# Optimization experiments

Measured on AMD Instinct MI355X. Metric: run time of the kernel, lower is better.

Reference implementation:

```python
import math
import jax, jax.numpy as jnp
import numpy as np

B, N, F, K = 4, 4096, 128, 32
EPS = 1e-8  # tsl.epsilon
TEMP0, TEMP_DECAY = 1.0, 0.99995


def setup_inputs() -> dict:
    key = jax.random.key(0)
    k1, k2, k3, k4 = jax.random.split(key, 4)
    emb = jax.random.normal(k1, (B, N, F), dtype=jnp.float32)
    adj = jax.random.uniform(k2, (B, N, N), dtype=jnp.float32)
    logits_param = jax.random.normal(k3, (N, K), dtype=jnp.float32)
    u = jax.random.uniform(k4, (B, N, K), dtype=jnp.float32, minval=1e-9, maxval=1.0)
    gumbel_noise = -jnp.log(-jnp.log(u))
    return {"emb": emb, "adj": adj, "logits_param": logits_param, "gumbel_noise": gumbel_noise}


def reference(emb, adj, logits_param, gumbel_noise):
    # temp decays on each get_temp() call in training mode (called twice per forward)
    t1 = max(TEMP0 * TEMP_DECAY, 0.05)
    t2 = max(t1 * TEMP_DECAY, 0.05)

    # ---- gumbel-softmax hard sample with straight-through estimator ----
    y_soft = jax.nn.softmax(logits_param[None] / t1 + gumbel_noise, axis=-1)  # [B,N,K]
    y_hard = jax.nn.one_hot(jnp.argmax(y_soft, axis=-1), K, dtype=y_soft.dtype)
    s_sample = jax.lax.stop_gradient(y_hard - y_soft) + y_soft + EPS  # [B,N,K]

    # ---- soft assignment for regularizers (unbatched [N,K]) ----
    s_soft = jax.nn.softmax(logits_param / t2, axis=-1)  # [N,K]

    # mincut_num = trace(s^T A s) per batch, without forming [K,K]
    As = jnp.einsum('bnm,mk->bnk', adj, s_soft)            # [B,N,K]
    mincut_num = jnp.einsum('nk,bnk->b', s_soft, As)       # [B]
    # mincut_den = trace(s^T D s): D is diag(deg) -> O(N*K) instead of diag_embed
    d_flat = adj.sum(axis=-1)                              # [B,N]
    mincut_den = jnp.einsum('bn,nk,nk->b', d_flat, s_soft, s_soft)
    mincut_loss = -jnp.mean(mincut_num / mincut_den)

    ss = s_soft.T @ s_soft                                 # [K,K]
    ortho_loss = jnp.linalg.norm(ss / jnp.linalg.norm(ss) - jnp.eye(K, dtype=ss.dtype) / math.sqrt(K))

    # ---- pooling ----
    out_emb = jnp.einsum('bnk,bnf->bkf', s_sample, emb)    # [B,K,F]
    As2 = jnp.einsum('bnm,bml->bnl', adj, s_sample)        # [B,N,K]
    out_adj = jnp.einsum('bnk,bnl->bkl', s_sample, As2)    # [B,K,K]

    out_adj = out_adj * (1.0 - jnp.eye(K, dtype=out_adj.dtype))  # zero diagonal
    d = jnp.sqrt(out_adj.sum(axis=-1, keepdims=True)) + EPS
    out_adj = out_adj / d / jnp.swapaxes(d, -1, -2)

    return out_emb, out_adj, s_sample, mincut_loss, ortho_loss
```

## Files before the change

kernel.cpp:

```cpp
#include <hip/hip_runtime.h>
#include <hip/hip_bf16.h>
#include <math.h>

#define B_ 4
#define N_ 4096
#define F_ 128
#define K_ 32
#define EPS_ 1e-8f

typedef __attribute__((ext_vector_type(8))) __bf16 bf16x8;
typedef __attribute__((ext_vector_type(4))) float f32x4;

#define WS_SSOFT   0
#define WS_SQ      131072
#define WS_SSP     135168
#define WS_WFS     200704
#define WS_WFH     266240
#define WS_OADJP   528384
#define WS_NUMDEN  1576960
#define WS_PEMB    1579008
#define WS_H       2627584

__global__ void k_pre(const float* __restrict__ logits, const float* __restrict__ gum,
                      float* __restrict__ s_soft, float* __restrict__ sq,
                      float* __restrict__ ssp, float* __restrict__ s_sample,
                      int* __restrict__ h, bf16x8* __restrict__ wfs,
                      bf16x8* __restrict__ wfh, float t1, float t2) {
  __shared__ float sl[64][33];
  __shared__ int hl[4][64];
  int t = threadIdx.x;
  int r = blockIdx.x;
  int n0 = r * 64;

  if (t < 64) {
    int n = n0 + t;
    float z[32];
    float mx = -1e30f;
    for (int k = 0; k < 32; ++k) { z[k] = logits[n*32+k] / t2; mx = fmaxf(mx, z[k]); }
    float s = 0.f;
    for (int k = 0; k < 32; ++k) { z[k] = expf(z[k]-mx); s += z[k]; }
    float sqa = 0.f;
    for (int k = 0; k < 32; ++k) {
      float v = z[k] / s;
      s_soft[n*32+k] = v;
      sl[t][k] = v;
      sqa += v*v;
    }
    sq[n] = sqa;
  }

  {
    int b = t >> 6, nn = t & 63;
    int n = n0 + nn;
    size_t i = (size_t)b * N_ + n;
    float z[32];
    float mx = -1e30f;
    for (int k = 0; k < 32; ++k) { z[k] = logits[n*32+k]/t1 + gum[i*32+k]; mx = fmaxf(mx, z[k]); }
    float s = 0.f;
    for (int k = 0; k < 32; ++k) { z[k] = expf(z[k]-mx); s += z[k]; }
    int am = 0; float best = -1.f;
    for (int k = 0; k < 32; ++k) { z[k] = z[k]/s; if (z[k] > best) { best = z[k]; am = k; } }
    for (int k = 0; k < 32; ++k) {
      float yh = (k==am) ? 1.f : 0.f;
      s_sample[i*32+k] = (yh - z[k]) + z[k] + EPS_;
    }
    h[i] = am;
    hl[b][nn] = am;
  }
  __syncthreads();

  for (int pp = 0; pp < 4; ++pp) {
    int p = pp*256 + t;
    int k = p >> 5, l = p & 31;
    float a = 0.f;
    for (int rr = 0; rr < 64; ++rr) a += sl[rr][k]*sl[rr][l];
    ssp[(size_t)r*1024 + p] = a;
  }

  {
    int lane = t & 63;
    int c = (t >> 6) & 1;
    int tts = t >> 7;
    int col = c*16 + (lane & 15);
    int lrow = tts*32 + (lane >> 4)*8;
    bf16x8 v;
    #pragma unroll
    for (int j = 0; j < 8; ++j) v[j] = (__bf16)sl[lrow+j][col];
    wfs[((size_t)(2*r + tts)*2 + c)*64 + lane] = v;
  }

  for (int it = 0; it < 4; ++it) {
    int p = it*256 + t;
    int lane = p & 63;
    int c = (p >> 6) & 1;
    int tts = (p >> 7) & 1;
    int b = p >> 8;
    int cc = c*16 + (lane & 15);
    int lrow = tts*32 + (lane >> 4)*8;
    bf16x8 v;
    #pragma unroll
    for (int j = 0; j < 8; ++j) v[j] = (__bf16)((hl[b][lrow+j] == cc) ? 1.f : 0.f);
    wfh[(((size_t)b*(N_/32) + 2*r + tts)*2 + c)*64 + lane] = v;
  }
}

#define NT(p) __builtin_nontemporal_load((const f32x4*)(p))

__launch_bounds__(256, 4)
__global__ void k_gemm(const float* __restrict__ adj, const float* __restrict__ emb,
                       const bf16x8* __restrict__ wfs, const bf16x8* __restrict__ wfh,
                       const float* __restrict__ s_soft, const float* __restrict__ sq,
                       const int* __restrict__ h, float* __restrict__ numden_p,
                       float* __restrict__ oadjp, float* __restrict__ pemb) {
  __shared__ float sh[4096];
  __shared__ float rn[4], rd[4];
  int t = threadIdx.x;
  int bid = blockIdx.x;

  if (bid < 256) {
    for (int i = t; i < 4096; i += 256) sh[i] = 0.f;
    __syncthreads();
    int b = bid >> 6;
    int n0 = (bid & 63) * 64;
    int f = t & 127, rr = t >> 7;
    for (int it = 0; it < 32; ++it) {
      int n = n0 + it*2 + rr;
      float v = emb[((size_t)b*N_ + n)*F_ + f];
      int hv = h[b*N_ + n];
      atomicAdd(&sh[hv*128 + f], v);
    }
    __syncthreads();
    for (int i = t; i < 4096; i += 256) pemb[(size_t)bid*4096 + i] = sh[i];
    return;
  }

  int gid = bid - 256;
  int w = t >> 6, l = t & 63;
  int lr = l & 15, lhi = l >> 4;
  int sp = gid & 7, r = (gid >> 3) & 31, b = gid >> 8;
  float* oal = sh;

  for (int i = t; i < 1024; i += 256) oal[i] = 0.f;
  __syncthreads();

  int row0 = r*128;
  int m0 = sp*512;
  int rowA = row0 + w*32 + lr;

  const float* pA0 = adj + (size_t)b*N_*N_ + (size_t)rowA*N_ + m0 + lhi*8;
  const float* pA1 = pA0 + (size_t)16*N_;
  const bf16x8* pws = wfs + (size_t)(m0 >> 5)*128 + l;
  const bf16x8* pwh = wfh + ((size_t)b*(N_/32) + (m0 >> 5))*128 + l;

  f32x4 acc00 = {0,0,0,0}, acc01 = {0,0,0,0}, acc02 = {0,0,0,0}, acc03 = {0,0,0,0};
  f32x4 acc10 = {0,0,0,0}, acc11 = {0,0,0,0}, acc12 = {0,0,0,0}, acc13 = {0,0,0,0};

  f32x4 a0lo = NT(pA0), a0hi = NT(pA0 + 4);
  f32x4 a1lo = NT(pA1), a1hi = NT(pA1 + 4);
  bf16x8 wc0 = pws[0], wc1 = pws[64], wc2 = pwh[0], wc3 = pwh[64];

  #pragma unroll 1
  for (int c = 0; c < 16; ++c) {
    f32x4 n0lo, n0hi, n1lo, n1hi;
    bf16x8 wn0, wn1, wn2, wn3;
    if (c < 15) {
      pA0 += 32; pA1 += 32; pws += 128; pwh += 128;
      n0lo = NT(pA0); n0hi = NT(pA0 + 4);
      n1lo = NT(pA1); n1hi = NT(pA1 + 4);
      wn0 = pws[0]; wn1 = pws[64]; wn2 = pwh[0]; wn3 = pwh[64];
    }
    bf16x8 fa0, fa1;
    #pragma unroll
    for (int j = 0; j < 4; ++j) {
      fa0[j]   = (__bf16)a0lo[j];
      fa0[j+4] = (__bf16)a0hi[j];
      fa1[j]   = (__bf16)a1lo[j];
      fa1[j+4] = (__bf16)a1hi[j];
    }
    acc00 = __builtin_amdgcn_mfma_f32_16x16x32_bf16(fa0, wc0, acc00, 0, 0, 0);
    acc01 = __builtin_amdgcn_mfma_f32_16x16x32_bf16(fa0, wc1, acc01, 0, 0, 0);
    acc02 = __builtin_amdgcn_mfma_f32_16x16x32_bf16(fa0, wc2, acc02, 0, 0, 0);
    acc03 = __builtin_amdgcn_mfma_f32_16x16x32_bf16(fa0, wc3, acc03, 0, 0, 0);
    acc10 = __builtin_amdgcn_mfma_f32_16x16x32_bf16(fa1, wc0, acc10, 0, 0, 0);
    acc11 = __builtin_amdgcn_mfma_f32_16x16x32_bf16(fa1, wc1, acc11, 0, 0, 0);
    acc12 = __builtin_amdgcn_mfma_f32_16x16x32_bf16(fa1, wc2, acc12, 0, 0, 0);
    acc13 = __builtin_amdgcn_mfma_f32_16x16x32_bf16(fa1, wc3, acc13, 0, 0, 0);
    if (c < 15) {
      a0lo = n0lo; a0hi = n0hi; a1lo = n1lo; a1hi = n1hi;
      wc0 = wn0; wc1 = wn1; wc2 = wn2; wc3 = wn3;
    }
  }

  float numacc = 0.f, denacc = 0.f;
  {
    f32x4 a0s[2] = {acc00, acc10}, a1s[2] = {acc01, acc11};
    f32x4 a2s[2] = {acc02, acc12}, a3s[2] = {acc03, acc13};
    int wrow0 = row0 + w*32;
    #pragma unroll
    for (int rt = 0; rt < 2; ++rt) {
      int rbase = wrow0 + rt*16 + lhi*4;
      #pragma unroll
      for (int i = 0; i < 4; ++i) {
        int row = rbase + i;
        float sqv = sq[row];
        int hv = h[b*N_ + row];
        numacc += a0s[rt][i] * s_soft[row*32 + lr];
        numacc += a1s[rt][i] * s_soft[row*32 + 16 + lr];
        float v2 = a2s[rt][i], v3 = a3s[rt][i];
        denacc += (v2 + v3) * sqv;
        atomicAdd(&oal[hv*32 + lr], v2);
        atomicAdd(&oal[hv*32 + 16 + lr], v3);
      }
    }
  }
  for (int off = 32; off; off >>= 1) {
    numacc += __shfl_down(numacc, off);
    denacc += __shfl_down(denacc, off);
  }
  if (l == 0) { rn[w] = numacc; rd[w] = denacc; }
  __syncthreads();
  if (t == 0) {
    numden_p[gid] = rn[0]+rn[1]+rn[2]+rn[3];
    numden_p[1024 + gid] = rd[0]+rd[1]+rd[2]+rd[3];
  }
  for (int i = t; i < 1024; i += 256) oadjp[(size_t)gid*1024 + i] = oal[i];
}

__global__ void k_post(const float* __restrict__ oadjp, const float* __restrict__ pemb,
                       const float* __restrict__ ndp, const float* __restrict__ ssp,
                       float* __restrict__ dout) {
  int blk = blockIdx.x;
  int t = threadIdx.x;
  if (blk < 64) {
    int i = blk*256 + t;
    int b = i >> 12, ii = i & 4095;
    float s = 0.f;
    const float* p = pemb + (size_t)(b*64)*4096 + ii;
    for (int j = 0; j < 64; ++j) s += p[(size_t)j*4096];
    dout[i] = s;
  } else if (blk < 68) {
    __shared__ float oal[1024];
    __shared__ float dsh[32];
    int b = blk - 64;
    float a0 = 0.f, a1 = 0.f, a2 = 0.f, a3 = 0.f;
    const float* p = oadjp + (size_t)b*256*1024 + t;
    for (int j = 0; j < 256; ++j) {
      a0 += p[0]; a1 += p[256]; a2 += p[512]; a3 += p[768];
      p += 1024;
    }
    oal[t] = a0; oal[t+256] = a1; oal[t+512] = a2; oal[t+768] = a3;
    __syncthreads();
    if (t < 32) {
      float s = 0.f;
      for (int l = 0; l < 32; ++l) if (l != t) s += oal[t*32+l];
      dsh[t] = sqrtf(s) + EPS_;
    }
    __syncthreads();
    for (int i = t; i < 1024; i += 256) {
      int k = i >> 5, l = i & 31;
      float v = (k == l) ? 0.f : oal[i] / (dsh[k] * dsh[l]);
      dout[16384 + b*1024 + i] = v;
    }
  } else {
    __shared__ float red[256];
    __shared__ float nd[8];
    if (t < 8) {
      int b = t & 3;
      const float* p = ndp + (t >> 2)*1024 + b*256;
      float s = 0.f;
      for (int j = 0; j < 256; ++j) s += p[j];
      nd[t] = s;
    }
    float v0 = 0.f, v1 = 0.f, v2 = 0.f, v3 = 0.f;
    for (int r = 0; r < 64; ++r) {
      const float* p = ssp + (size_t)r*1024 + t;
      v0 += p[0]; v1 += p[256]; v2 += p[512]; v3 += p[768];
    }
    float a = v0*v0 + v1*v1 + v2*v2 + v3*v3;
    red[t] = a; __syncthreads();
    for (int s2 = 128; s2; s2 >>= 1) { if (t < s2) red[t] += red[t+s2]; __syncthreads(); }
    float fro = sqrtf(red[0]);
    __syncthreads();
    float inv = 1.f / fro;
    float dk = (float)(1.0 / sqrt(32.0));
    float c = 0.f;
    {
      float w;
      int p0 = t, p1 = t+256, p2 = t+512, p3 = t+768;
      w = v0*inv - (((p0>>5)==(p0&31)) ? dk : 0.f); c += w*w;
      w = v1*inv - (((p1>>5)==(p1&31)) ? dk : 0.f); c += w*w;
      w = v2*inv - (((p2>>5)==(p2&31)) ? dk : 0.f); c += w*w;
      w = v3*inv - (((p3>>5)==(p3&31)) ? dk : 0.f); c += w*w;
    }
    red[t] = c; __syncthreads();
    for (int s2 = 128; s2; s2 >>= 1) { if (t < s2) red[t] += red[t+s2]; __syncthreads(); }
    if (t == 0) {
      dout[544769] = sqrtf(red[0]);
      float s = 0.f;
      for (int b = 0; b < 4; ++b) s += nd[b] / nd[4+b];
      dout[544768] = -s*0.25f;
    }
  }
}

extern "C" void kernel_launch(void* const* d_in, const int* in_sizes, int n_in,
                              void* d_out, int out_size, void* d_ws, size_t ws_size,
                              hipStream_t stream) {
  const float* emb    = (const float*)d_in[0];
  const float* adj    = (const float*)d_in[1];
  const float* logits = (const float*)d_in[2];
  const float* gum    = (const float*)d_in[3];
  float* out = (float*)d_out;
  float* ws  = (float*)d_ws;

  float t1 = 0.99995f;
  float t2 = (float)(0.99995 * 0.99995);

  float* s_soft = ws + WS_SSOFT;
  float* sq     = ws + WS_SQ;
  float* ssp    = ws + WS_SSP;
  bf16x8* wfs   = (bf16x8*)(ws + WS_WFS);
  bf16x8* wfh   = (bf16x8*)(ws + WS_WFH);
  float* oadjp  = ws + WS_OADJP;
  float* ndp    = ws + WS_NUMDEN;
  float* pemb   = ws + WS_PEMB;
  int* hbuf     = (int*)(ws + WS_H);

  k_pre  <<<64, 256, 0, stream>>>(logits, gum, s_soft, sq, ssp, out + 20480, hbuf, wfs, wfh, t1, t2);
  k_gemm <<<1280, 256, 0, stream>>>(adj, emb, wfs, wfh, s_soft, sq, hbuf, ndp, oadjp, pemb);
  k_post <<<69, 256, 0, stream>>>(oadjp, pemb, ndp, ssp, out);
}
```

Before: 416.8 us.

## Stage adj tiles through swizzled LDS with full-row blocks and split-K across waves

The GEMM blocks now each own 32 full rows of adj. Threads load 32 contiguous floats per row with coalesced nontemporal loads, convert them to bf16, and write them into an XOR-swizzled shared-memory tile. Each wave then reads its K-slice of that tile as MFMA fragments. This replaces the earlier scheme, where each lane fetched 8-float fragments straight from global memory across 8 column splits. The aim is better-coalesced, deeper-prefetched streaming of the large adj matrix and fewer partial outputs to reduce in k_post. In exchange it adds two barriers per step, more registers (launch bounds lowered to 3), and fewer blocks (512 GEMM blocks instead of 1024).

Result: slower. 448.3 us (+7.6%).

```diff
diff --git a/kernel.cpp b/kernel.cpp
--- a/kernel.cpp
+++ b/kernel.cpp
@@ -10,6 +10,7 @@
 
 typedef __attribute__((ext_vector_type(8))) __bf16 bf16x8;
 typedef __attribute__((ext_vector_type(4))) float f32x4;
+typedef __attribute__((ext_vector_type(4))) unsigned int u32x4;
 
 #define WS_SSOFT   0
 #define WS_SQ      131072
@@ -106,88 +107,106 @@
 
 #define NT(p) __builtin_nontemporal_load((const f32x4*)(p))
 
-__launch_bounds__(256, 4)
+union PK2 { __bf16 h[2]; unsigned int u; };
+union FRU { u32x4 q; bf16x8 v; };
+
+static __device__ __forceinline__ unsigned int pk2(float a, float b) {
+  PK2 x; x.h[0] = (__bf16)a; x.h[1] = (__bf16)b; return x.u;
+}
+
+__launch_bounds__(256, 3)
 __global__ void k_gemm(const float* __restrict__ adj, const float* __restrict__ emb,
                        const bf16x8* __restrict__ wfs, const bf16x8* __restrict__ wfh,
                        const float* __restrict__ s_soft, const float* __restrict__ sq,
                        const int* __restrict__ h, float* __restrict__ numden_p,
                        float* __restrict__ oadjp, float* __restrict__ pemb) {
-  __shared__ float sh[4096];
+  __shared__ u32x4 la[32*32];
+  __shared__ float oal[1024];
   __shared__ float rn[4], rd[4];
   int t = threadIdx.x;
   int bid = blockIdx.x;
 
-  if (bid < 256) {
-    for (int i = t; i < 4096; i += 256) sh[i] = 0.f;
-    __syncthreads();
-    int b = bid >> 6;
-    int n0 = (bid & 63) * 64;
+  if (bid >= 512) {
+    __shared__ float accl[4096];
+    int ob = bid - 512;
+    for (int i = t; i < 4096; i += 256) accl[i] = 0.f;
+    __syncthreads();
+    int b = ob >> 6;
+    int n0 = (ob & 63) * 64;
     int f = t & 127, rr = t >> 7;
     for (int it = 0; it < 32; ++it) {
       int n = n0 + it*2 + rr;
       float v = emb[((size_t)b*N_ + n)*F_ + f];
       int hv = h[b*N_ + n];
-      atomicAdd(&sh[hv*128 + f], v);
-    }
-    __syncthreads();
-    for (int i = t; i < 4096; i += 256) pemb[(size_t)bid*4096 + i] = sh[i];
+      atomicAdd(&accl[hv*128 + f], v);
+    }
+    __syncthreads();
+    for (int i = t; i < 4096; i += 256) pemb[(size_t)ob*4096 + i] = accl[i];
     return;
   }
 
-  int gid = bid - 256;
   int w = t >> 6, l = t & 63;
   int lr = l & 15, lhi = l >> 4;
-  int sp = gid & 7, r = (gid >> 3) & 31, b = gid >> 8;
-  float* oal = sh;
+  int b = bid >> 7, rb = bid & 127;
+  int row0 = rb * 32;
 
   for (int i = t; i < 1024; i += 256) oal[i] = 0.f;
-  __syncthreads();
-
-  int row0 = r*128;
-  int m0 = sp*512;
-  int rowA = row0 + w*32 + lr;
-
-  const float* pA0 = adj + (size_t)b*N_*N_ + (size_t)rowA*N_ + m0 + lhi*8;
-  const float* pA1 = pA0 + (size_t)16*N_;
-  const bf16x8* pws = wfs + (size_t)(m0 >> 5)*128 + l;
-  const bf16x8* pwh = wfh + ((size_t)b*(N_/32) + (m0 >> 5))*128 + l;
+
+  int srow = t >> 3;
+  const float* pA = adj + (size_t)b*N_*N_ + (size_t)(row0 + srow)*N_ + (t & 7)*32;
 
   f32x4 acc00 = {0,0,0,0}, acc01 = {0,0,0,0}, acc02 = {0,0,0,0}, acc03 = {0,0,0,0};
   f32x4 acc10 = {0,0,0,0}, acc11 = {0,0,0,0}, acc12 = {0,0,0,0}, acc13 = {0,0,0,0};
 
-  f32x4 a0lo = NT(pA0), a0hi = NT(pA0 + 4);
-  f32x4 a1lo = NT(pA1), a1hi = NT(pA1 + 4);
-  bf16x8 wc0 = pws[0], wc1 = pws[64], wc2 = pwh[0], wc3 = pwh[64];
-
-  #pragma unroll 1
-  for (int c = 0; c < 16; ++c) {
-    f32x4 n0lo, n0hi, n1lo, n1hi;
-    bf16x8 wn0, wn1, wn2, wn3;
-    if (c < 15) {
-      pA0 += 32; pA1 += 32; pws += 128; pwh += 128;
-      n0lo = NT(pA0); n0hi = NT(pA0 + 4);
-      n1lo = NT(pA1); n1hi = NT(pA1 + 4);
-      wn0 = pws[0]; wn1 = pws[64]; wn2 = pwh[0]; wn3 = pwh[64];
-    }
-    bf16x8 fa0, fa1;
+  f32x4 ar[2][8];
+  #pragma unroll
+  for (int i = 0; i < 8; ++i) ar[0][i] = NT(pA + i*4);
+
+  #pragma unroll 2
+  for (int s = 0; s < 16; ++s) {
+    int cur = s & 1;
+    if (s < 15) {
+      #pragma unroll
+      for (int i = 0; i < 8; ++i) ar[cur^1][i] = NT(pA + (s+1)*256 + i*4);
+    }
+    if (s > 0) __syncthreads();
+    {
+      int gbase = srow*32 + (t & 7)*4;
+      int swz = srow & 7;
+      #pragma unroll
+      for (int q = 0; q < 4; ++q) {
+        u32x4 val;
+        #pragma unroll
+        for (int m = 0; m < 4; ++m) {
+          int j = q*4 + m;
+          val[m] = pk2(ar[cur][j>>1][(j&1)*2], ar[cur][j>>1][(j&1)*2+1]);
+        }
+        la[(gbase + q) ^ swz] = val;
+      }
+    }
+    __syncthreads();
     #pragma unroll
-    for (int j = 0; j < 4; ++j) {
-      fa0[j]   = (__bf16)a0lo[j];
-      fa0[j+4] = (__bf16)a0hi[j];
-      fa1[j]   = (__bf16)a1lo[j];
-      fa1[j+4] = (__bf16)a1hi[j];
-    }
-    acc00 = __builtin_amdgcn_mfma_f32_16x16x32_bf16(fa0, wc0, acc00, 0, 0, 0);
-    acc01 = __builtin_amdgcn_mfma_f32_16x16x32_bf16(fa0, wc1, acc01, 0, 0, 0);
-    acc02 = __builtin_amdgcn_mfma_f32_16x16x32_bf16(fa0, wc2, acc02, 0, 0, 0);
-    acc03 = __builtin_amdgcn_mfma_f32_16x16x32_bf16(fa0, wc3, acc03, 0, 0, 0);
-    acc10 = __builtin_amdgcn_mfma_f32_16x16x32_bf16(fa1, wc0, acc10, 0, 0, 0);
-    acc11 = __builtin_amdgcn_mfma_f32_16x16x32_bf16(fa1, wc1, acc11, 0, 0, 0);
-    acc12 = __builtin_amdgcn_mfma_f32_16x16x32_bf16(fa1, wc2, acc12, 0, 0, 0);
-    acc13 = __builtin_amdgcn_mfma_f32_16x16x32_bf16(fa1, wc3, acc13, 0, 0, 0);
-    if (c < 15) {
-      a0lo = n0lo; a0hi = n0hi; a1lo = n1lo; a1hi = n1hi;
-      wc0 = wn0; wc1 = wn1; wc2 = wn2; wc3 = wn3;
+    for (int st = 0; st < 2; ++st) {
+      int c32 = s*8 + w*2 + st;
+      bf16x8 wf0 = wfs[((size_t)c32*2 + 0)*64 + l];
+      bf16x8 wf1 = wfs[((size_t)c32*2 + 1)*64 + l];
+      bf16x8 wh0 = wfh[(((size_t)b*(N_/32) + c32)*2 + 0)*64 + l];
+      bf16x8 wh1 = wfh[(((size_t)b*(N_/32) + c32)*2 + 1)*64 + l];
+      FRU fa0, fa1;
+      {
+        int row = lr;
+        fa0.q = la[(row*32 + w*8 + st*4 + lhi) ^ (row & 7)];
+        row = 16 + lr;
+        fa1.q = la[(row*32 + w*8 + st*4 + lhi) ^ (row & 7)];
+      }
+      acc00 = __builtin_amdgcn_mfma_f32_16x16x32_bf16(fa0.v, wf0, acc00, 0, 0, 0);
+      acc01 = __builtin_amdgcn_mfma_f32_16x16x32_bf16(fa0.v, wf1, acc01, 0, 0, 0);
+      acc02 = __builtin_amdgcn_mfma_f32_16x16x32_bf16(fa0.v, wh0, acc02, 0, 0, 0);
+      acc03 = __builtin_amdgcn_mfma_f32_16x16x32_bf16(fa0.v, wh1, acc03, 0, 0, 0);
+      acc10 = __builtin_amdgcn_mfma_f32_16x16x32_bf16(fa1.v, wf0, acc10, 0, 0, 0);
+      acc11 = __builtin_amdgcn_mfma_f32_16x16x32_bf16(fa1.v, wf1, acc11, 0, 0, 0);
+      acc12 = __builtin_amdgcn_mfma_f32_16x16x32_bf16(fa1.v, wh0, acc12, 0, 0, 0);
+      acc13 = __builtin_amdgcn_mfma_f32_16x16x32_bf16(fa1.v, wh1, acc13, 0, 0, 0);
     }
   }
 
@@ -195,10 +214,9 @@
   {
     f32x4 a0s[2] = {acc00, acc10}, a1s[2] = {acc01, acc11};
     f32x4 a2s[2] = {acc02, acc12}, a3s[2] = {acc03, acc13};
-    int wrow0 = row0 + w*32;
     #pragma unroll
     for (int rt = 0; rt < 2; ++rt) {
-      int rbase = wrow0 + rt*16 + lhi*4;
+      int rbase = row0 + rt*16 + lhi*4;
       #pragma unroll
       for (int i = 0; i < 4; ++i) {
         int row = rbase + i;
@@ -220,10 +238,10 @@
   if (l == 0) { rn[w] = numacc; rd[w] = denacc; }
   __syncthreads();
   if (t == 0) {
-    numden_p[gid] = rn[0]+rn[1]+rn[2]+rn[3];
-    numden_p[1024 + gid] = rd[0]+rd[1]+rd[2]+rd[3];
-  }
-  for (int i = t; i < 1024; i += 256) oadjp[(size_t)gid*1024 + i] = oal[i];
+    numden_p[bid] = rn[0]+rn[1]+rn[2]+rn[3];
+    numden_p[1024 + bid] = rd[0]+rd[1]+rd[2]+rd[3];
+  }
+  for (int i = t; i < 1024; i += 256) oadjp[(size_t)bid*1024 + i] = oal[i];
 }
 
 __global__ void k_post(const float* __restrict__ oadjp, const float* __restrict__ pemb,
@@ -243,8 +261,8 @@
     __shared__ float dsh[32];
     int b = blk - 64;
     float a0 = 0.f, a1 = 0.f, a2 = 0.f, a3 = 0.f;
-    const float* p = oadjp + (size_t)b*256*1024 + t;
-    for (int j = 0; j < 256; ++j) {
+    const float* p = oadjp + (size_t)b*128*1024 + t;
+    for (int j = 0; j < 128; ++j) {
       a0 += p[0]; a1 += p[256]; a2 += p[512]; a3 += p[768];
       p += 1024;
     }
@@ -266,9 +284,9 @@
     __shared__ float nd[8];
     if (t < 8) {
       int b = t & 3;
-      const float* p = ndp + (t >> 2)*1024 + b*256;
+      const float* p = ndp + (t >> 2)*1024 + b*128;
       float s = 0.f;
-      for (int j = 0; j < 256; ++j) s += p[j];
+      for (int j = 0; j < 128; ++j) s += p[j];
       nd[t] = s;
     }
     float v0 = 0.f, v1 = 0.f, v2 = 0.f, v3 = 0.f;
@@ -327,6 +345,6 @@
   int* hbuf     = (int*)(ws + WS_H);
 
   k_pre  <<<64, 256, 0, stream>>>(logits, gum, s_soft, sq, ssp, out + 20480, hbuf, wfs, wfh, t1, t2);
-  k_gemm <<<1280, 256, 0, stream>>>(adj, emb, wfs, wfh, s_soft, sq, hbuf, ndp, oadjp, pemb);
+  k_gemm <<<768, 256, 0, stream>>>(adj, emb, wfs, wfh, s_soft, sq, hbuf, ndp, oadjp, pemb);
   k_post <<<69, 256, 0, stream>>>(oadjp, pemb, ndp, ssp, out);
 }
```
